# Performance work log

Measured on AMD Instinct MI355X. Metric: run time of the kernel, lower is better.

Reference implementation:

```python
import jax, jax.numpy as jnp
import numpy as np

N_NODES = 100000
N_EDGES = 3200000


def _gcn_conv(x, src, dst, W, b, n_nodes):
    # PyG GCNConv: out = D^{-1/2} (A + I) D^{-1/2} X W + b
    h = x @ W  # [N, out]
    # degree of (A + I) counted at targets (symmetric graph assumption as in PyG norm)
    deg = jax.ops.segment_sum(jnp.ones_like(dst, dtype=h.dtype), dst, num_segments=n_nodes)
    dinv = jnp.where(deg > 0, jax.lax.rsqrt(deg), 0.0)
    norm = dinv[src] * dinv[dst]  # [E_total]
    msg = h[src] * norm[:, None]  # gather + normalize  [E_total, out]
    out = jax.ops.segment_sum(msg, dst, num_segments=n_nodes)  # scatter-add
    return out + b


def setup_inputs() -> dict:
    key = jax.random.key(0)
    k1, k2, k3, k4 = jax.random.split(key, 4)
    x = jax.random.normal(k1, (N_NODES, 1), dtype=jnp.float32)
    edge_index = jax.random.randint(k2, (2, N_EDGES), 0, N_NODES, dtype=jnp.int64)
    W1 = jax.random.normal(k3, (1, 64), dtype=jnp.float32) * (1.0 / np.sqrt(1.0))
    b1 = jnp.zeros((64,), dtype=jnp.float32)
    W2 = jax.random.normal(k4, (64, 2), dtype=jnp.float32) * (1.0 / np.sqrt(64.0))
    b2 = jnp.zeros((2,), dtype=jnp.float32)
    return {"x": x, "edge_index": edge_index, "W1": W1, "b1": b1, "W2": W2, "b2": b2}


def reference(x, edge_index, W1, b1, W2, b2):
    n = x.shape[0]
    # add self-loops as GCNConv does by default
    loops = jnp.arange(n, dtype=edge_index.dtype)
    src = jnp.concatenate([edge_index[0], loops])
    dst = jnp.concatenate([edge_index[1], loops])
    h = _gcn_conv(x, src, dst, W1, b1, n)
    h = jax.nn.relu(h)
    h = _gcn_conv(h, src, dst, W2, b2, n)
    h = jax.nn.log_softmax(h, axis=1)
    out = jnp.mean(h, axis=0)
    return out[None, :]  # [1, 2]
```

## Files before the change

kernel.cpp:

```cpp
#include <hip/hip_runtime.h>


#define TPB 512
#define SORT_BLK 256
#define BSHIFT 7
#define BNODES 128
#define MAXBUCK 1024
#define BSTRIDE 6144


__global__ __launch_bounds__(TPB) void k_sort(const int* __restrict__ ei, int E, int epb,
                                              int nbuck, int* __restrict__ gcur,
                                              unsigned* __restrict__ packed) {
    __shared__ int h[MAXBUCK];
    for (int b = threadIdx.x; b < nbuck; b += TPB) h[b] = 0;
    __syncthreads();
    const int4* d4 = (const int4*)(ei + E);
    int nq = epb >> 2;
    int q0 = blockIdx.x * nq;
    for (int j = threadIdx.x; j < nq; j += TPB) {
        int q = q0 + j;
        int e = q << 2;
        if (e + 3 < E) {
            int4 v = d4[q];
            atomicAdd(&h[v.x >> BSHIFT], 1);
            atomicAdd(&h[v.y >> BSHIFT], 1);
            atomicAdd(&h[v.z >> BSHIFT], 1);
            atomicAdd(&h[v.w >> BSHIFT], 1);
        } else {
            for (int k = 0; k < 4; ++k)
                if (e + k < E) atomicAdd(&h[(ei + E)[e + k] >> BSHIFT], 1);
        }
    }
    __syncthreads();
    for (int b = threadIdx.x; b < nbuck; b += TPB) {
        int c = h[b];
        h[b] = c ? atomicAdd(&gcur[b], c) : 0;
    }
    __syncthreads();
    const int4* s4 = (const int4*)ei;
    for (int j = threadIdx.x; j < nq; j += TPB) {
        int q = q0 + j;
        int e = q << 2;
        if (e + 3 < E) {
            int4 vs = s4[q];
            int4 vd = d4[q];
            int b, p;
            b = vd.x >> BSHIFT; p = atomicAdd(&h[b], 1);
            packed[b * BSTRIDE + p] = ((unsigned)(vd.x & (BNODES - 1)) << 17) | (unsigned)vs.x;
            b = vd.y >> BSHIFT; p = atomicAdd(&h[b], 1);
            packed[b * BSTRIDE + p] = ((unsigned)(vd.y & (BNODES - 1)) << 17) | (unsigned)vs.y;
            b = vd.z >> BSHIFT; p = atomicAdd(&h[b], 1);
            packed[b * BSTRIDE + p] = ((unsigned)(vd.z & (BNODES - 1)) << 17) | (unsigned)vs.z;
            b = vd.w >> BSHIFT; p = atomicAdd(&h[b], 1);
            packed[b * BSTRIDE + p] = ((unsigned)(vd.w & (BNODES - 1)) << 17) | (unsigned)vs.w;
        } else {
            for (int k = 0; k < 4; ++k) {
                int ee = e + k;
                if (ee < E) {
                    int s = ei[ee], d = ei[E + ee];
                    int b = d >> BSHIFT;
                    int p = atomicAdd(&h[b], 1);
                    packed[b * BSTRIDE + p] = ((unsigned)(d & (BNODES - 1)) << 17) | (unsigned)s;
                }
            }
        }
    }
}


__global__ __launch_bounds__(TPB) void k_deg_u(const unsigned* __restrict__ packed,
                                               const int* __restrict__ gcur,
                                               const float* __restrict__ x,
                                               float* __restrict__ dinv,
                                               float* __restrict__ u, int N) {
    __shared__ int cnt[8][BNODES];
    for (int k = threadIdx.x; k < 8 * BNODES; k += TPB) ((int*)cnt)[k] = 0;
    __syncthreads();
    int b = blockIdx.x;
    int sz = gcur[b];
    const unsigned* base = packed + (size_t)b * BSTRIDE;
    const uint4* base4 = (const uint4*)base;
    int wv = threadIdx.x >> 6;
    int nq4 = sz >> 2;
    int half = nq4 >> 1;
    for (int j = threadIdx.x; j < half; j += TPB) {
        uint4 p = base4[j];
        uint4 q = base4[j + half];
        atomicAdd(&cnt[wv][(p.x >> 17) & 127], 1);
        atomicAdd(&cnt[wv][(p.y >> 17) & 127], 1);
        atomicAdd(&cnt[wv][(p.z >> 17) & 127], 1);
        atomicAdd(&cnt[wv][(p.w >> 17) & 127], 1);
        atomicAdd(&cnt[wv][(q.x >> 17) & 127], 1);
        atomicAdd(&cnt[wv][(q.y >> 17) & 127], 1);
        atomicAdd(&cnt[wv][(q.z >> 17) & 127], 1);
        atomicAdd(&cnt[wv][(q.w >> 17) & 127], 1);
    }
    for (int j = half * 8 + threadIdx.x; j < sz; j += TPB) {
        unsigned p = base[j];
        atomicAdd(&cnt[wv][(p >> 17) & 127], 1);
    }
    __syncthreads();
    if (threadIdx.x < BNODES) {
        int t = threadIdx.x;
        int node = (b << BSHIFT) + t;
        if (node < N) {
            int deg = 0;
            #pragma unroll
            for (int c = 0; c < 8; ++c) deg += cnt[c][t];
            float di = rsqrtf((float)(deg + 1));
            dinv[node] = di;
            u[node] = di * x[node];
        }
    }
}


__global__ __launch_bounds__(TPB) void k_agg1(const unsigned* __restrict__ packed,
                                              const int* __restrict__ gcur,
                                              const float* __restrict__ dinv,
                                              const float* __restrict__ u,
                                              const float* __restrict__ W1,
                                              const float* __restrict__ b1,
                                              const float* __restrict__ W2,
                                              float2* __restrict__ w, int N) {
    __shared__ float acc[8][BNODES];
    __shared__ float sW1[64], sb1[64], sW2[128];
    if (threadIdx.x < 64) { sW1[threadIdx.x] = W1[threadIdx.x]; sb1[threadIdx.x] = b1[threadIdx.x]; }
    else if (threadIdx.x >= 64 && threadIdx.x < 192) sW2[threadIdx.x - 64] = W2[threadIdx.x - 64];
    for (int k = threadIdx.x; k < 8 * BNODES; k += TPB) ((float*)acc)[k] = 0.f;
    __syncthreads();
    int b = blockIdx.x;
    int sz = gcur[b];
    const unsigned* base = packed + (size_t)b * BSTRIDE;
    const uint4* base4 = (const uint4*)base;
    int wv = threadIdx.x >> 6;
    int nq4 = sz >> 2;
    int half = nq4 >> 1;
    for (int j = threadIdx.x; j < half; j += TPB) {
        uint4 p = base4[j];
        uint4 q = base4[j + half];
        float v0 = u[p.x & 0x1FFFF];
        float v1 = u[p.y & 0x1FFFF];
        float v2 = u[p.z & 0x1FFFF];
        float v3 = u[p.w & 0x1FFFF];
        float v4 = u[q.x & 0x1FFFF];
        float v5 = u[q.y & 0x1FFFF];
        float v6 = u[q.z & 0x1FFFF];
        float v7 = u[q.w & 0x1FFFF];
        atomicAdd(&acc[wv][(p.x >> 17) & 127], v0);
        atomicAdd(&acc[wv][(p.y >> 17) & 127], v1);
        atomicAdd(&acc[wv][(p.z >> 17) & 127], v2);
        atomicAdd(&acc[wv][(p.w >> 17) & 127], v3);
        atomicAdd(&acc[wv][(q.x >> 17) & 127], v4);
        atomicAdd(&acc[wv][(q.y >> 17) & 127], v5);
        atomicAdd(&acc[wv][(q.z >> 17) & 127], v6);
        atomicAdd(&acc[wv][(q.w >> 17) & 127], v7);
    }
    for (int j = half * 8 + threadIdx.x; j < sz; j += TPB) {
        unsigned p = base[j];
        atomicAdd(&acc[wv][(p >> 17) & 127], u[p & 0x1FFFF]);
    }
    __syncthreads();
    if (threadIdx.x < BNODES) {
        int t = threadIdx.x;
        int node = (b << BSHIFT) + t;
        if (node < N) {
            float s = 0.f;
            #pragma unroll
            for (int c = 0; c < 8; ++c) s += acc[c][t];
            float di = dinv[node];
            float sv = di * (s + u[node]);
            float z0 = 0.f, z1 = 0.f;
            #pragma unroll
            for (int j = 0; j < 64; ++j) {
                float h = fmaxf(fmaf(sv, sW1[j], sb1[j]), 0.f);
                z0 = fmaf(h, sW2[2 * j], z0);
                z1 = fmaf(h, sW2[2 * j + 1], z1);
            }
            w[node] = make_float2(di * z0, di * z1);
        }
    }
}


__global__ __launch_bounds__(TPB) void k_agg2(const unsigned* __restrict__ packed,
                                              const int* __restrict__ gcur,
                                              const float* __restrict__ dinv,
                                              const float2* __restrict__ w,
                                              const float* __restrict__ b2,
                                              float* __restrict__ accum, int N) {
    __shared__ float accx[8][BNODES], accy[8][BNODES];
    for (int k = threadIdx.x; k < 8 * BNODES; k += TPB) {
        ((float*)accx)[k] = 0.f;
        ((float*)accy)[k] = 0.f;
    }
    __syncthreads();
    int b = blockIdx.x;
    int sz = gcur[b];
    const unsigned* base = packed + (size_t)b * BSTRIDE;
    const uint4* base4 = (const uint4*)base;
    int wv = threadIdx.x >> 6;
    int nq4 = sz >> 2;
    int half = nq4 >> 1;
    for (int j = threadIdx.x; j < half; j += TPB) {
        uint4 p = base4[j];
        uint4 q = base4[j + half];
        float2 v0 = w[p.x & 0x1FFFF];
        float2 v1 = w[p.y & 0x1FFFF];
        float2 v2 = w[p.z & 0x1FFFF];
        float2 v3 = w[p.w & 0x1FFFF];
        float2 v4 = w[q.x & 0x1FFFF];
        float2 v5 = w[q.y & 0x1FFFF];
        float2 v6 = w[q.z & 0x1FFFF];
        float2 v7 = w[q.w & 0x1FFFF];
        int l0 = (p.x >> 17) & 127, l1 = (p.y >> 17) & 127;
        int l2 = (p.z >> 17) & 127, l3 = (p.w >> 17) & 127;
        int l4 = (q.x >> 17) & 127, l5 = (q.y >> 17) & 127;
        int l6 = (q.z >> 17) & 127, l7 = (q.w >> 17) & 127;
        atomicAdd(&accx[wv][l0], v0.x); atomicAdd(&accy[wv][l0], v0.y);
        atomicAdd(&accx[wv][l1], v1.x); atomicAdd(&accy[wv][l1], v1.y);
        atomicAdd(&accx[wv][l2], v2.x); atomicAdd(&accy[wv][l2], v2.y);
        atomicAdd(&accx[wv][l3], v3.x); atomicAdd(&accy[wv][l3], v3.y);
        atomicAdd(&accx[wv][l4], v4.x); atomicAdd(&accy[wv][l4], v4.y);
        atomicAdd(&accx[wv][l5], v5.x); atomicAdd(&accy[wv][l5], v5.y);
        atomicAdd(&accx[wv][l6], v6.x); atomicAdd(&accy[wv][l6], v6.y);
        atomicAdd(&accx[wv][l7], v7.x); atomicAdd(&accy[wv][l7], v7.y);
    }
    for (int j = half * 8 + threadIdx.x; j < sz; j += TPB) {
        unsigned p = base[j];
        float2 v = w[p & 0x1FFFF];
        int l = (p >> 17) & 127;
        atomicAdd(&accx[wv][l], v.x);
        atomicAdd(&accy[wv][l], v.y);
    }
    __syncthreads();
    float l0 = 0.f, l1 = 0.f;
    if (threadIdx.x < BNODES) {
        int t = threadIdx.x;
        int node = (b << BSHIFT) + t;
        if (node < N) {
            float sx = 0.f, sy = 0.f;
            #pragma unroll
            for (int c = 0; c < 8; ++c) { sx += accx[c][t]; sy += accy[c][t]; }
            float di = dinv[node];
            float2 wi = w[node];
            float a0 = di * (sx + wi.x) + b2[0];
            float a1 = di * (sy + wi.y) + b2[1];
            float m = fmaxf(a0, a1);
            float lse = m + logf(expf(a0 - m) + expf(a1 - m));
            l0 = a0 - lse;
            l1 = a1 - lse;
        }
    }
    #pragma unroll
    for (int off = 32; off > 0; off >>= 1) {
        l0 += __shfl_down(l0, off, 64);
        l1 += __shfl_down(l1, off, 64);
    }
    __shared__ float s0[TPB / 64], s1[TPB / 64];
    int wid = threadIdx.x >> 6, lane = threadIdx.x & 63;
    if (lane == 0) { s0[wid] = l0; s1[wid] = l1; }
    __syncthreads();
    if (threadIdx.x == 0) {
        float t0 = 0.f, t1 = 0.f;
        #pragma unroll
        for (int k = 0; k < TPB / 64; ++k) { t0 += s0[k]; t1 += s1[k]; }
        accum[2 * b]     = t0;
        accum[2 * b + 1] = t1;
    }
}


#define RTPB 1024
__global__ __launch_bounds__(RTPB) void k_reduce_final(const float* __restrict__ accum,
                                                       int nb, float* __restrict__ out,
                                                       float invN) {
    float t0 = 0.f, t1 = 0.f;
    for (int i = threadIdx.x; i < nb; i += RTPB) {
        t0 += accum[2 * i];
        t1 += accum[2 * i + 1];
    }
    #pragma unroll
    for (int off = 32; off > 0; off >>= 1) {
        t0 += __shfl_down(t0, off, 64);
        t1 += __shfl_down(t1, off, 64);
    }
    __shared__ float s0[RTPB / 64], s1[RTPB / 64];
    int wid = threadIdx.x >> 6, lane = threadIdx.x & 63;
    if (lane == 0) { s0[wid] = t0; s1[wid] = t1; }
    __syncthreads();
    if (threadIdx.x == 0) {
        float a = 0.f, b = 0.f;
        #pragma unroll
        for (int k = 0; k < RTPB / 64; ++k) { a += s0[k]; b += s1[k]; }
        out[0] = a * invN;
        out[1] = b * invN;
    }
}

__global__ void k_finalize(const float* __restrict__ accum, float* __restrict__ out, float invN) {
    out[0] = accum[0] * invN;
    out[1] = accum[1] * invN;
}


#define FTPB 256
__global__ void k_hist(const int* __restrict__ dst, int E, int* __restrict__ deg) {
    int e = blockIdx.x * FTPB + threadIdx.x;
    if (e < E) atomicAdd(&deg[dst[e]], 1);
}
__global__ void k_dinv_u(const int* __restrict__ deg, const float* __restrict__ x,
                         float* __restrict__ dinv, float* __restrict__ u, int N) {
    int i = blockIdx.x * FTPB + threadIdx.x;
    if (i < N) {
        float di = rsqrtf((float)(deg[i] + 1));
        dinv[i] = di;
        u[i] = di * x[i];
    }
}
__global__ void k_scatter1(const int* __restrict__ ei, int E,
                           const float* __restrict__ u, float* __restrict__ t) {
    int e = blockIdx.x * FTPB + threadIdx.x;
    if (e < E) atomicAdd(&t[ei[E + e]], u[ei[e]]);
}
__global__ void k_node_mid_fb(const float* __restrict__ dinv, const float* __restrict__ u,
                              const float* __restrict__ t,
                              const float* __restrict__ W1, const float* __restrict__ b1,
                              const float* __restrict__ W2, float2* __restrict__ w, int N) {
    __shared__ float sW1[64], sb1[64], sW2[128];
    if (threadIdx.x < 64) { sW1[threadIdx.x] = W1[threadIdx.x]; sb1[threadIdx.x] = b1[threadIdx.x]; }
    if (threadIdx.x < 128) sW2[threadIdx.x] = W2[threadIdx.x];
    __syncthreads();
    int i = blockIdx.x * FTPB + threadIdx.x;
    if (i < N) {
        float di = dinv[i];
        float s = di * (t[i] + u[i]);
        float z0 = 0.f, z1 = 0.f;
        #pragma unroll
        for (int j = 0; j < 64; ++j) {
            float h = fmaxf(fmaf(s, sW1[j], sb1[j]), 0.f);
            z0 = fmaf(h, sW2[2 * j], z0);
            z1 = fmaf(h, sW2[2 * j + 1], z1);
        }
        w[i] = make_float2(di * z0, di * z1);
    }
}
__global__ void k_scatter2(const int* __restrict__ ei, int E,
                           const float2* __restrict__ w, float* __restrict__ acc) {
    int e = blockIdx.x * FTPB + threadIdx.x;
    if (e < E) {
        float2 ws = w[ei[e]];
        int d = ei[E + e];
        atomicAdd(&acc[2 * d], ws.x);
        atomicAdd(&acc[2 * d + 1], ws.y);
    }
}
__global__ void k_node_out_fb(const float* __restrict__ dinv, const float2* __restrict__ w,
                              const float2* __restrict__ acc, const float* __restrict__ b2,
                              float* __restrict__ accum, int N) {
    int i = blockIdx.x * FTPB + threadIdx.x;
    float l0 = 0.f, l1 = 0.f;
    if (i < N) {
        float di = dinv[i];
        float2 a = acc[i];
        float2 ww = w[i];
        float a0 = di * (a.x + ww.x) + b2[0];
        float a1 = di * (a.y + ww.y) + b2[1];
        float m = fmaxf(a0, a1);
        float lse = m + logf(expf(a0 - m) + expf(a1 - m));
        l0 = a0 - lse;
        l1 = a1 - lse;
    }
    #pragma unroll
    for (int off = 32; off > 0; off >>= 1) {
        l0 += __shfl_down(l0, off, 64);
        l1 += __shfl_down(l1, off, 64);
    }
    __shared__ float s0[FTPB / 64], s1[FTPB / 64];
    int wid = threadIdx.x >> 6, lane = threadIdx.x & 63;
    if (lane == 0) { s0[wid] = l0; s1[wid] = l1; }
    __syncthreads();
    if (threadIdx.x == 0) {
        float t0 = 0.f, t1 = 0.f;
        #pragma unroll
        for (int k = 0; k < FTPB / 64; ++k) { t0 += s0[k]; t1 += s1[k]; }
        atomicAdd(&accum[0], t0);
        atomicAdd(&accum[1], t1);
    }
}

extern "C" void kernel_launch(void* const* d_in, const int* in_sizes, int n_in,
                              void* d_out, int out_size, void* d_ws, size_t ws_size,
                              hipStream_t stream) {
    const float* x  = (const float*)d_in[0];
    const int*   ei = (const int*)d_in[1];
    const float* W1 = (const float*)d_in[2];
    const float* b1 = (const float*)d_in[3];
    const float* W2 = (const float*)d_in[4];
    const float* b2 = (const float*)d_in[5];
    float* out = (float*)d_out;

    const int N = in_sizes[0];
    const int E = in_sizes[1] / 2;
    const int nbuck = (N + BNODES - 1) >> BSHIFT;
    const int gridN = (N + FTPB - 1) / FTPB;
    const int gridE = (E + FTPB - 1) / FTPB;

    size_t offPacked = 0;
    size_t offW      = offPacked + (size_t)nbuck * BSTRIDE * 4;
    size_t offDinv   = offW + (size_t)N * 8;
    size_t offU      = offDinv + (size_t)N * 4;
    size_t offGcur   = offU + (size_t)N * 4;
    size_t offAccum  = offGcur + (size_t)nbuck * 4;
    size_t need      = offAccum + (size_t)2 * nbuck * 4;

    if (ws_size >= need && nbuck <= MAXBUCK && N <= (1 << 17)) {
        unsigned* packed = (unsigned*)((char*)d_ws + offPacked);
        float2*   w      = (float2*)((char*)d_ws + offW);
        float*    dinv   = (float*)((char*)d_ws + offDinv);
        float*    u      = (float*)((char*)d_ws + offU);
        int*      gcur   = (int*)((char*)d_ws + offGcur);
        float*    accum  = (float*)((char*)d_ws + offAccum);

        hipMemsetAsync(gcur, 0, (size_t)nbuck * 4, stream);

        int epb = (((E + SORT_BLK - 1) / SORT_BLK) + 3) & ~3;

        k_sort<<<SORT_BLK, TPB, 0, stream>>>(ei, E, epb, nbuck, gcur, packed);
        k_deg_u<<<nbuck, TPB, 0, stream>>>(packed, gcur, x, dinv, u, N);
        k_agg1<<<nbuck, TPB, 0, stream>>>(packed, gcur, dinv, u, W1, b1, W2, w, N);
        k_agg2<<<nbuck, TPB, 0, stream>>>(packed, gcur, dinv, (const float2*)w, b2, accum, N);
        k_reduce_final<<<1, RTPB, 0, stream>>>(accum, nbuck, out, 1.0f / (float)N);
    } else {
        int*   deg   = (int*)d_ws;
        float* t     = (float*)(deg + N);
        float* acc   = t + N;
        float* accum = acc + 2 * N;
        float* dinv  = accum + 2;
        float* u     = dinv + N;
        float2* w    = (float2*)(u + N);
        hipMemsetAsync(d_ws, 0, (size_t)(4 * N + 2) * sizeof(float), stream);
        k_hist<<<gridE, FTPB, 0, stream>>>(ei + E, E, deg);
        k_dinv_u<<<gridN, FTPB, 0, stream>>>(deg, x, dinv, u, N);
        k_scatter1<<<gridE, FTPB, 0, stream>>>(ei, E, u, t);
        k_node_mid_fb<<<gridN, FTPB, 0, stream>>>(dinv, u, t, W1, b1, W2, w, N);
        k_scatter2<<<gridE, FTPB, 0, stream>>>(ei, E, w, acc);
        k_node_out_fb<<<gridN, FTPB, 0, stream>>>(dinv, w, (const float2*)acc, b2, accum, N);
        k_finalize<<<1, 64, 0, stream>>>(accum, out, 1.0f / (float)N);
    }
}
```

Measured before the change: 188.2 us.

## Build per-bucket CSR in degree kernel and aggregate without LDS atomics

The degree kernel now prefix-sums the per-node counts, writes per-node row pointers, and reorders each bucket's edge list by destination through an LDS staging buffer, writing it back in place. Both aggregation kernels then walk each node's contiguous source list with four lanes per node and a shuffle reduction, instead of doing float LDS atomics into eight per-wave partial accumulators. This removes the atomic contention in the two aggregation passes, at the cost of a heavier CSR kernel (extra pass, large LDS stage, global rewrite). Neighbor-count imbalance across nodes can also leave lanes idle.

```diff
diff --git a/kernel.cpp b/kernel.cpp
--- a/kernel.cpp
+++ b/kernel.cpp
@@ -69,17 +69,20 @@
 }
 
 
-__global__ __launch_bounds__(TPB) void k_deg_u(const unsigned* __restrict__ packed,
-                                               const int* __restrict__ gcur,
-                                               const float* __restrict__ x,
-                                               float* __restrict__ dinv,
-                                               float* __restrict__ u, int N) {
+__global__ __launch_bounds__(TPB) void k_csr(unsigned* __restrict__ packed,
+                                             const int* __restrict__ gcur,
+                                             const float* __restrict__ x,
+                                             float* __restrict__ dinv,
+                                             float* __restrict__ u,
+                                             int* __restrict__ rptr, int N) {
     __shared__ int cnt[8][BNODES];
+    __shared__ int eptr[BNODES];
+    __shared__ unsigned stage[BSTRIDE];
     for (int k = threadIdx.x; k < 8 * BNODES; k += TPB) ((int*)cnt)[k] = 0;
     __syncthreads();
     int b = blockIdx.x;
     int sz = gcur[b];
-    const unsigned* base = packed + (size_t)b * BSTRIDE;
+    unsigned* base = packed + (size_t)b * BSTRIDE;
     const uint4* base4 = (const uint4*)base;
     int wv = threadIdx.x >> 6;
     int nq4 = sz >> 2;
@@ -101,171 +104,146 @@
         atomicAdd(&cnt[wv][(p >> 17) & 127], 1);
     }
     __syncthreads();
+    int tot = 0;
+    if (threadIdx.x < BNODES) {
+        #pragma unroll
+        for (int c = 0; c < 8; ++c) tot += cnt[c][threadIdx.x];
+        eptr[threadIdx.x] = tot;
+    }
+    __syncthreads();
+    for (int d = 1; d < BNODES; d <<= 1) {
+        int add = 0;
+        if (threadIdx.x < BNODES && threadIdx.x >= d) add = eptr[threadIdx.x - d];
+        __syncthreads();
+        if (threadIdx.x < BNODES) eptr[threadIdx.x] += add;
+        __syncthreads();
+    }
     if (threadIdx.x < BNODES) {
         int t = threadIdx.x;
+        int ex = eptr[t] - tot;
+        int run = ex;
+        #pragma unroll
+        for (int c = 0; c < 8; ++c) { int v = cnt[c][t]; cnt[c][t] = run; run += v; }
+        rptr[b * BNODES + t] = ex;
         int node = (b << BSHIFT) + t;
         if (node < N) {
-            int deg = 0;
-            #pragma unroll
-            for (int c = 0; c < 8; ++c) deg += cnt[c][t];
-            float di = rsqrtf((float)(deg + 1));
+            float di = rsqrtf((float)(tot + 1));
             dinv[node] = di;
             u[node] = di * x[node];
         }
     }
-}
-
-
-__global__ __launch_bounds__(TPB) void k_agg1(const unsigned* __restrict__ packed,
+    __syncthreads();
+    for (int j = threadIdx.x; j < half; j += TPB) {
+        uint4 p = base4[j];
+        uint4 q = base4[j + half];
+        int pos;
+        pos = atomicAdd(&cnt[wv][(p.x >> 17) & 127], 1); stage[pos] = p.x & 0x1FFFF;
+        pos = atomicAdd(&cnt[wv][(p.y >> 17) & 127], 1); stage[pos] = p.y & 0x1FFFF;
+        pos = atomicAdd(&cnt[wv][(p.z >> 17) & 127], 1); stage[pos] = p.z & 0x1FFFF;
+        pos = atomicAdd(&cnt[wv][(p.w >> 17) & 127], 1); stage[pos] = p.w & 0x1FFFF;
+        pos = atomicAdd(&cnt[wv][(q.x >> 17) & 127], 1); stage[pos] = q.x & 0x1FFFF;
+        pos = atomicAdd(&cnt[wv][(q.y >> 17) & 127], 1); stage[pos] = q.y & 0x1FFFF;
+        pos = atomicAdd(&cnt[wv][(q.z >> 17) & 127], 1); stage[pos] = q.z & 0x1FFFF;
+        pos = atomicAdd(&cnt[wv][(q.w >> 17) & 127], 1); stage[pos] = q.w & 0x1FFFF;
+    }
+    for (int j = half * 8 + threadIdx.x; j < sz; j += TPB) {
+        unsigned p = base[j];
+        int pos = atomicAdd(&cnt[wv][(p >> 17) & 127], 1);
+        stage[pos] = p & 0x1FFFF;
+    }
+    __syncthreads();
+    for (int k = threadIdx.x; k < sz; k += TPB) base[k] = stage[k];
+}
+
+
+__global__ __launch_bounds__(TPB) void k_agg1(const unsigned* __restrict__ sorted,
                                               const int* __restrict__ gcur,
+                                              const int* __restrict__ rptr,
                                               const float* __restrict__ dinv,
                                               const float* __restrict__ u,
                                               const float* __restrict__ W1,
                                               const float* __restrict__ b1,
                                               const float* __restrict__ W2,
                                               float2* __restrict__ w, int N) {
-    __shared__ float acc[8][BNODES];
     __shared__ float sW1[64], sb1[64], sW2[128];
+    __shared__ int sptr[BNODES + 1];
+    int b = blockIdx.x;
     if (threadIdx.x < 64) { sW1[threadIdx.x] = W1[threadIdx.x]; sb1[threadIdx.x] = b1[threadIdx.x]; }
-    else if (threadIdx.x >= 64 && threadIdx.x < 192) sW2[threadIdx.x - 64] = W2[threadIdx.x - 64];
-    for (int k = threadIdx.x; k < 8 * BNODES; k += TPB) ((float*)acc)[k] = 0.f;
-    __syncthreads();
-    int b = blockIdx.x;
-    int sz = gcur[b];
-    const unsigned* base = packed + (size_t)b * BSTRIDE;
-    const uint4* base4 = (const uint4*)base;
-    int wv = threadIdx.x >> 6;
-    int nq4 = sz >> 2;
-    int half = nq4 >> 1;
-    for (int j = threadIdx.x; j < half; j += TPB) {
-        uint4 p = base4[j];
-        uint4 q = base4[j + half];
-        float v0 = u[p.x & 0x1FFFF];
-        float v1 = u[p.y & 0x1FFFF];
-        float v2 = u[p.z & 0x1FFFF];
-        float v3 = u[p.w & 0x1FFFF];
-        float v4 = u[q.x & 0x1FFFF];
-        float v5 = u[q.y & 0x1FFFF];
-        float v6 = u[q.z & 0x1FFFF];
-        float v7 = u[q.w & 0x1FFFF];
-        atomicAdd(&acc[wv][(p.x >> 17) & 127], v0);
-        atomicAdd(&acc[wv][(p.y >> 17) & 127], v1);
-        atomicAdd(&acc[wv][(p.z >> 17) & 127], v2);
-        atomicAdd(&acc[wv][(p.w >> 17) & 127], v3);
-        atomicAdd(&acc[wv][(q.x >> 17) & 127], v4);
-        atomicAdd(&acc[wv][(q.y >> 17) & 127], v5);
-        atomicAdd(&acc[wv][(q.z >> 17) & 127], v6);
-        atomicAdd(&acc[wv][(q.w >> 17) & 127], v7);
-    }
-    for (int j = half * 8 + threadIdx.x; j < sz; j += TPB) {
-        unsigned p = base[j];
-        atomicAdd(&acc[wv][(p >> 17) & 127], u[p & 0x1FFFF]);
-    }
-    __syncthreads();
-    if (threadIdx.x < BNODES) {
-        int t = threadIdx.x;
-        int node = (b << BSHIFT) + t;
-        if (node < N) {
-            float s = 0.f;
-            #pragma unroll
-            for (int c = 0; c < 8; ++c) s += acc[c][t];
-            float di = dinv[node];
-            float sv = di * (s + u[node]);
-            float z0 = 0.f, z1 = 0.f;
-            #pragma unroll
-            for (int j = 0; j < 64; ++j) {
-                float h = fmaxf(fmaf(sv, sW1[j], sb1[j]), 0.f);
-                z0 = fmaf(h, sW2[2 * j], z0);
-                z1 = fmaf(h, sW2[2 * j + 1], z1);
-            }
-            w[node] = make_float2(di * z0, di * z1);
+    else if (threadIdx.x < 192) sW2[threadIdx.x - 64] = W2[threadIdx.x - 64];
+    if (threadIdx.x < BNODES) sptr[threadIdx.x] = rptr[b * BNODES + threadIdx.x];
+    if (threadIdx.x == 0) sptr[BNODES] = gcur[b];
+    __syncthreads();
+    int t = threadIdx.x >> 2, k = threadIdx.x & 3;
+    const unsigned* base = sorted + (size_t)b * BSTRIDE;
+    int s0 = sptr[t], s1 = sptr[t + 1];
+    float s = 0.f;
+    for (int j = s0 + k; j < s1; j += 4) s += u[base[j] & 0x1FFFF];
+    s += __shfl_xor(s, 1, 64);
+    s += __shfl_xor(s, 2, 64);
+    int node = (b << BSHIFT) + t;
+    if (k == 0 && node < N) {
+        float di = dinv[node];
+        float sv = di * (s + u[node]);
+        float z0 = 0.f, z1 = 0.f;
+        #pragma unroll
+        for (int j = 0; j < 64; ++j) {
+            float h = fmaxf(fmaf(sv, sW1[j], sb1[j]), 0.f);
+            z0 = fmaf(h, sW2[2 * j], z0);
+            z1 = fmaf(h, sW2[2 * j + 1], z1);
         }
-    }
-}
-
-
-__global__ __launch_bounds__(TPB) void k_agg2(const unsigned* __restrict__ packed,
+        w[node] = make_float2(di * z0, di * z1);
+    }
+}
+
+
+__global__ __launch_bounds__(TPB) void k_agg2(const unsigned* __restrict__ sorted,
                                               const int* __restrict__ gcur,
+                                              const int* __restrict__ rptr,
                                               const float* __restrict__ dinv,
                                               const float2* __restrict__ w,
                                               const float* __restrict__ b2,
                                               float* __restrict__ accum, int N) {
-    __shared__ float accx[8][BNODES], accy[8][BNODES];
-    for (int k = threadIdx.x; k < 8 * BNODES; k += TPB) {
-        ((float*)accx)[k] = 0.f;
-        ((float*)accy)[k] = 0.f;
-    }
-    __syncthreads();
+    __shared__ int sptr[BNODES + 1];
     int b = blockIdx.x;
-    int sz = gcur[b];
-    const unsigned* base = packed + (size_t)b * BSTRIDE;
-    const uint4* base4 = (const uint4*)base;
-    int wv = threadIdx.x >> 6;
-    int nq4 = sz >> 2;
-    int half = nq4 >> 1;
-    for (int j = threadIdx.x; j < half; j += TPB) {
-        uint4 p = base4[j];
-        uint4 q = base4[j + half];
-        float2 v0 = w[p.x & 0x1FFFF];
-        float2 v1 = w[p.y & 0x1FFFF];
-        float2 v2 = w[p.z & 0x1FFFF];
-        float2 v3 = w[p.w & 0x1FFFF];
-        float2 v4 = w[q.x & 0x1FFFF];
-        float2 v5 = w[q.y & 0x1FFFF];
-        float2 v6 = w[q.z & 0x1FFFF];
-        float2 v7 = w[q.w & 0x1FFFF];
-        int l0 = (p.x >> 17) & 127, l1 = (p.y >> 17) & 127;
-        int l2 = (p.z >> 17) & 127, l3 = (p.w >> 17) & 127;
-        int l4 = (q.x >> 17) & 127, l5 = (q.y >> 17) & 127;
-        int l6 = (q.z >> 17) & 127, l7 = (q.w >> 17) & 127;
-        atomicAdd(&accx[wv][l0], v0.x); atomicAdd(&accy[wv][l0], v0.y);
-        atomicAdd(&accx[wv][l1], v1.x); atomicAdd(&accy[wv][l1], v1.y);
-        atomicAdd(&accx[wv][l2], v2.x); atomicAdd(&accy[wv][l2], v2.y);
-        atomicAdd(&accx[wv][l3], v3.x); atomicAdd(&accy[wv][l3], v3.y);
-        atomicAdd(&accx[wv][l4], v4.x); atomicAdd(&accy[wv][l4], v4.y);
-        atomicAdd(&accx[wv][l5], v5.x); atomicAdd(&accy[wv][l5], v5.y);
-        atomicAdd(&accx[wv][l6], v6.x); atomicAdd(&accy[wv][l6], v6.y);
-        atomicAdd(&accx[wv][l7], v7.x); atomicAdd(&accy[wv][l7], v7.y);
-    }
-    for (int j = half * 8 + threadIdx.x; j < sz; j += TPB) {
-        unsigned p = base[j];
-        float2 v = w[p & 0x1FFFF];
-        int l = (p >> 17) & 127;
-        atomicAdd(&accx[wv][l], v.x);
-        atomicAdd(&accy[wv][l], v.y);
-    }
-    __syncthreads();
+    if (threadIdx.x < BNODES) sptr[threadIdx.x] = rptr[b * BNODES + threadIdx.x];
+    if (threadIdx.x == 0) sptr[BNODES] = gcur[b];
+    __syncthreads();
+    int t = threadIdx.x >> 2, k = threadIdx.x & 3;
+    const unsigned* base = sorted + (size_t)b * BSTRIDE;
+    int s0 = sptr[t], s1 = sptr[t + 1];
+    float sx = 0.f, sy = 0.f;
+    for (int j = s0 + k; j < s1; j += 4) {
+        float2 v = w[base[j] & 0x1FFFF];
+        sx += v.x;
+        sy += v.y;
+    }
+    sx += __shfl_xor(sx, 1, 64); sx += __shfl_xor(sx, 2, 64);
+    sy += __shfl_xor(sy, 1, 64); sy += __shfl_xor(sy, 2, 64);
+    int node = (b << BSHIFT) + t;
     float l0 = 0.f, l1 = 0.f;
-    if (threadIdx.x < BNODES) {
-        int t = threadIdx.x;
-        int node = (b << BSHIFT) + t;
-        if (node < N) {
-            float sx = 0.f, sy = 0.f;
-            #pragma unroll
-            for (int c = 0; c < 8; ++c) { sx += accx[c][t]; sy += accy[c][t]; }
-            float di = dinv[node];
-            float2 wi = w[node];
-            float a0 = di * (sx + wi.x) + b2[0];
-            float a1 = di * (sy + wi.y) + b2[1];
-            float m = fmaxf(a0, a1);
-            float lse = m + logf(expf(a0 - m) + expf(a1 - m));
-            l0 = a0 - lse;
-            l1 = a1 - lse;
-        }
+    if (k == 0 && node < N) {
+        float di = dinv[node];
+        float2 wi = w[node];
+        float a0 = di * (sx + wi.x) + b2[0];
+        float a1 = di * (sy + wi.y) + b2[1];
+        float m = fmaxf(a0, a1);
+        float lse = m + logf(expf(a0 - m) + expf(a1 - m));
+        l0 = a0 - lse;
+        l1 = a1 - lse;
     }
     #pragma unroll
     for (int off = 32; off > 0; off >>= 1) {
         l0 += __shfl_down(l0, off, 64);
         l1 += __shfl_down(l1, off, 64);
     }
-    __shared__ float s0[TPB / 64], s1[TPB / 64];
+    __shared__ float r0[TPB / 64], r1[TPB / 64];
     int wid = threadIdx.x >> 6, lane = threadIdx.x & 63;
-    if (lane == 0) { s0[wid] = l0; s1[wid] = l1; }
+    if (lane == 0) { r0[wid] = l0; r1[wid] = l1; }
     __syncthreads();
     if (threadIdx.x == 0) {
         float t0 = 0.f, t1 = 0.f;
         #pragma unroll
-        for (int k = 0; k < TPB / 64; ++k) { t0 += s0[k]; t1 += s1[k]; }
+        for (int kk = 0; kk < TPB / 64; ++kk) { t0 += r0[kk]; t1 += r1[kk]; }
         accum[2 * b]     = t0;
         accum[2 * b + 1] = t1;
     }
@@ -413,7 +391,8 @@
     size_t offU      = offDinv + (size_t)N * 4;
     size_t offGcur   = offU + (size_t)N * 4;
     size_t offAccum  = offGcur + (size_t)nbuck * 4;
-    size_t need      = offAccum + (size_t)2 * nbuck * 4;
+    size_t offRptr   = offAccum + (size_t)2 * nbuck * 4;
+    size_t need      = offRptr + (size_t)nbuck * BNODES * 4;
 
     if (ws_size >= need && nbuck <= MAXBUCK && N <= (1 << 17)) {
         unsigned* packed = (unsigned*)((char*)d_ws + offPacked);
@@ -422,15 +401,16 @@
         float*    u      = (float*)((char*)d_ws + offU);
         int*      gcur   = (int*)((char*)d_ws + offGcur);
         float*    accum  = (float*)((char*)d_ws + offAccum);
+        int*      rptr   = (int*)((char*)d_ws + offRptr);
 
         hipMemsetAsync(gcur, 0, (size_t)nbuck * 4, stream);
 
         int epb = (((E + SORT_BLK - 1) / SORT_BLK) + 3) & ~3;
 
         k_sort<<<SORT_BLK, TPB, 0, stream>>>(ei, E, epb, nbuck, gcur, packed);
-        k_deg_u<<<nbuck, TPB, 0, stream>>>(packed, gcur, x, dinv, u, N);
-        k_agg1<<<nbuck, TPB, 0, stream>>>(packed, gcur, dinv, u, W1, b1, W2, w, N);
-        k_agg2<<<nbuck, TPB, 0, stream>>>(packed, gcur, dinv, (const float2*)w, b2, accum, N);
+        k_csr<<<nbuck, TPB, 0, stream>>>(packed, gcur, x, dinv, u, rptr, N);
+        k_agg1<<<nbuck, TPB, 0, stream>>>(packed, gcur, rptr, dinv, u, W1, b1, W2, w, N);
+        k_agg2<<<nbuck, TPB, 0, stream>>>(packed, gcur, rptr, dinv, (const float2*)w, b2, accum, N);
         k_reduce_final<<<1, RTPB, 0, stream>>>(accum, nbuck, out, 1.0f / (float)N);
     } else {
         int*   deg   = (int*)d_ws;
```

After: 164.8 us. 1.14x faster.
